# Kernel tuning notes

Measured on AMD Instinct MI355X. Metric: run time of the kernel, lower is better.

The kernel has to match this reference:

```python
import jax, jax.numpy as jnp
import numpy as np

EPS = 1e-6
NUM_HEADS = 12


def _layernorm(x, eps=EPS):
    m = jnp.mean(x, axis=-1, keepdims=True)
    v = jnp.var(x, axis=-1, keepdims=True)
    return (x - m) * jax.lax.rsqrt(v + eps)


def _rmsnorm(x, w, eps=EPS):
    ms = jnp.mean(jnp.square(x), axis=-1, keepdims=True)
    return x * jax.lax.rsqrt(ms + eps) * w


def _rope_interleaved(x, cos, sin):
    # x: [B, L, H, hd]; cos/sin: [L, hd//2]; is_neox_style=False (interleaved pairs)
    x1 = x[..., 0::2]
    x2 = x[..., 1::2]
    c = cos[None, :, None, :]
    s = sin[None, :, None, :]
    o1 = x1 * c - x2 * s
    o2 = x1 * s + x2 * c
    return jnp.stack([o1, o2], axis=-1).reshape(x.shape)


def _attention(q, k, v, mask=None):
    # q: [B, Lq, H, hd], k/v: [B, Lk, H, hd]
    hd = q.shape[-1]
    scale = 1.0 / jnp.sqrt(jnp.asarray(hd, q.dtype))
    scores = jnp.einsum('blhd,bmhd->bhlm', q, k) * scale
    if mask is not None:
        scores = jnp.where(mask[None, None], scores, jnp.finfo(scores.dtype).min)
    p = jax.nn.softmax(scores, axis=-1)
    return jnp.einsum('bhlm,bmhd->blhd', p, v)


def setup_inputs() -> dict:
    key = jax.random.key(0)
    B, F, FS, D, FF, LC = 1, 2, 1560, 1536, 8960, 512
    L = F * FS
    hd = D // NUM_HEADS
    ks = jax.random.split(key, 32)
    i = iter(range(32))
    n = lambda shape, s=0.02: jax.random.normal(ks[next(i)], shape, jnp.float32) * s
    inp = {
        'hidden_states': n((B, L, D), 1.0),
        'encoder_hidden_states': n((B, LC, D), 1.0),
        'temb': n((B, F, 6, D), 1.0),
    }
    pos = jnp.arange(L, dtype=jnp.float32)
    inv = 1.0 / (10000.0 ** (jnp.arange(hd // 2, dtype=jnp.float32) / (hd // 2)))
    ang = pos[:, None] * inv[None, :]
    inp['cos'] = jnp.cos(ang)
    inp['sin'] = jnp.sin(ang)
    fidx = jnp.arange(L) // FS
    inp['attn_mask'] = fidx[:, None] >= fidx[None, :]  # frame-level block-causal
    # params
    inp['sst'] = n((1, 6, D), 1.0 / np.sqrt(D))
    for name in ['wq', 'wk', 'wv', 'wo']:
        inp[name] = n((D, D))
    for name in ['bq', 'bk', 'bv', 'bo']:
        inp[name] = jnp.zeros((D,), jnp.float32)
    inp['nq_w'] = jnp.ones((D,), jnp.float32)
    inp['nk_w'] = jnp.ones((D,), jnp.float32)
    inp['ln2_g'] = jnp.ones((D,), jnp.float32)
    inp['ln2_b'] = jnp.zeros((D,), jnp.float32)
    for name in ['cwq', 'cwk', 'cwv', 'cwo']:
        inp[name] = n((D, D))
    for name in ['cbq', 'cbk', 'cbv', 'cbo']:
        inp[name] = jnp.zeros((D,), jnp.float32)
    inp['cnq_w'] = jnp.ones((D,), jnp.float32)
    inp['cnk_w'] = jnp.ones((D,), jnp.float32)
    inp['w1'] = n((D, FF))
    inp['b1'] = jnp.zeros((FF,), jnp.float32)
    inp['w2'] = n((FF, D))
    inp['b2'] = jnp.zeros((D,), jnp.float32)
    return inp


def reference(hidden_states, encoder_hidden_states, temb, cos, sin, attn_mask,
              sst, wq, bq, wk, bk, wv, bv, wo, bo, nq_w, nk_w, ln2_g, ln2_b,
              cwq, cbq, cwk, cbk, cwv, cbv, cwo, cbo, cnq_w, cnk_w,
              w1, b1, w2, b2):
    B, L, D = hidden_states.shape
    F = temb.shape[1]
    FS = L // F
    H = NUM_HEADS
    hd = D // H

    e = sst[:, None] + temb  # [B, F, 6, D]
    shift_msa, scale_msa, gate_msa = e[:, :, 0], e[:, :, 1], e[:, :, 2]
    c_shift, c_scale, c_gate = e[:, :, 3], e[:, :, 4], e[:, :, 5]

    # --- self attention ---
    nh = _layernorm(hidden_states).reshape(B, F, FS, D)
    nh = (nh * (1.0 + scale_msa[:, :, None]) + shift_msa[:, :, None]).reshape(B, L, D)
    q = _rmsnorm(nh @ wq + bq, nq_w).reshape(B, L, H, hd)
    k = _rmsnorm(nh @ wk + bk, nk_w).reshape(B, L, H, hd)
    v = (nh @ wv + bv).reshape(B, L, H, hd)
    q = _rope_interleaved(q, cos, sin)
    k = _rope_interleaved(k, cos, sin)
    attn_out = _attention(q, k, v, attn_mask).reshape(B, L, D) @ wo + bo

    h = hidden_states + (attn_out.reshape(B, F, FS, D) * gate_msa[:, :, None]).reshape(B, L, D)
    norm_h = _layernorm(h) * ln2_g + ln2_b  # null shift/scale

    # --- cross attention ---
    LC = encoder_hidden_states.shape[1]
    cq = _rmsnorm(norm_h @ cwq + cbq, cnq_w).reshape(B, L, H, hd)
    ck = _rmsnorm(encoder_hidden_states @ cwk + cbk, cnk_w).reshape(B, LC, H, hd)
    cv = (encoder_hidden_states @ cwv + cbv).reshape(B, LC, H, hd)
    cross_out = _attention(cq, ck, cv).reshape(B, L, D) @ cwo + cbo

    h = h + cross_out  # gate = 1
    norm_h = _layernorm(h).reshape(B, F, FS, D)
    norm_h = (norm_h * (1.0 + c_scale[:, :, None]) + c_shift[:, :, None]).reshape(B, L, D)

    # --- ffn ---
    ff = jax.nn.gelu(norm_h @ w1 + b1, approximate=True) @ w2 + b2
    h = h + (ff.reshape(B, F, FS, D) * c_gate[:, :, None]).reshape(B, L, D)
    return h
```

## Files before the change

kernel.cpp:

```cpp
#include <hip/hip_runtime.h>
#include <hip/hip_bf16.h>
#include <math.h>

typedef __bf16 bf16;
typedef __bf16 bf16x8 __attribute__((ext_vector_type(8)));
typedef float  f32x4  __attribute__((ext_vector_type(4)));
typedef unsigned int u32;

#define DMODEL 1536
#define NHEADS 12
#define HD 128
#define HDH 64

__device__ __forceinline__ void async16(const void* g, void* l) {
  __builtin_amdgcn_global_load_lds((const __attribute__((address_space(1))) u32*)g,
                                   (__attribute__((address_space(3))) u32*)l, 16, 0, 0);
}

__device__ inline void block_reduce2(float& a, float& b) {
  __shared__ float sa[4], sb[4];
  #pragma unroll
  for (int off = 32; off; off >>= 1) {
    a += __shfl_xor(a, off);
    b += __shfl_xor(b, off);
  }
  int w = threadIdx.x >> 6;
  if ((threadIdx.x & 63) == 0) { sa[w] = a; sb[w] = b; }
  __syncthreads();
  a = sa[0] + sa[1] + sa[2] + sa[3];
  b = sb[0] + sb[1] + sb[2] + sb[3];
  __syncthreads();
}

__global__ __launch_bounds__(256)
void ln_kernel(const float* __restrict__ X, bf16* __restrict__ Y,
               const float* __restrict__ sst, const float* __restrict__ temb,
               const float* __restrict__ g, const float* __restrict__ bvec,
               int jshift, int jscale, int FS, int mode)
{
  int row = blockIdx.x;
  const float* x = X + (size_t)row * DMODEL;
  float v[6];
  float s1 = 0.f, s2 = 0.f;
  #pragma unroll
  for (int i = 0; i < 6; i++) {
    float t = x[threadIdx.x + i * 256];
    v[i] = t; s1 += t; s2 += t * t;
  }
  block_reduce2(s1, s2);
  float mean = s1 * (1.f / DMODEL);
  float var  = s2 * (1.f / DMODEL) - mean * mean;
  float rs = rsqrtf(var + 1e-6f);
  int f = row / FS;
  bf16* y = Y + (size_t)row * DMODEL;
  #pragma unroll
  for (int i = 0; i < 6; i++) {
    int d = threadIdx.x + i * 256;
    float t = (v[i] - mean) * rs;
    float o;
    if (mode == 0) {
      float sc = sst[jscale * DMODEL + d] + temb[(f * 6 + jscale) * DMODEL + d];
      float sh = sst[jshift * DMODEL + d] + temb[(f * 6 + jshift) * DMODEL + d];
      o = t * (1.f + sc) + sh;
    } else {
      o = t * g[d] + bvec[d];
    }
    y[d] = (bf16)o;
  }
}

__global__ __launch_bounds__(256)
void rms_rope_kernel(const float* __restrict__ P, int S, long long MN,
                     const bf16* __restrict__ Xb, int RS, int CO,
                     const float* __restrict__ bias, bf16* __restrict__ Y,
                     const float* __restrict__ w,
                     const float* __restrict__ cosb, const float* __restrict__ sinb,
                     int dorope, float oscale)
{
  __shared__ float rowbuf[DMODEL];
  int row = blockIdx.x;
  float v[6];
  float s2 = 0.f, dummy = 0.f;
  if (Xb) {
    const bf16* x = Xb + (size_t)row * RS + CO;
    #pragma unroll
    for (int i = 0; i < 6; i++) {
      int d = threadIdx.x + i * 256;
      float t = (float)x[d];
      v[i] = t; rowbuf[d] = t; s2 += t * t;
    }
  } else {
    const float* x = P + (size_t)row * RS + CO;
    #pragma unroll
    for (int i = 0; i < 6; i++) {
      int d = threadIdx.x + i * 256;
      float t = bias[d];
      for (int s = 0; s < S; s++) t += x[(size_t)s * MN + d];
      v[i] = t; rowbuf[d] = t; s2 += t * t;
    }
  }
  __syncthreads();
  block_reduce2(s2, dummy);
  float rs = rsqrtf(s2 * (1.f / DMODEL) + 1e-6f) * oscale;
  bf16* y = Y + (size_t)row * DMODEL;
  if (dorope) {
    #pragma unroll
    for (int i = 0; i < 3; i++) {
      int p = threadIdx.x + i * 256;
      int d0 = 2 * p, d1 = 2 * p + 1;
      float y0 = rowbuf[d0] * rs * w[d0];
      float y1 = rowbuf[d1] * rs * w[d1];
      int ih = p & 63;
      float c = cosb[(size_t)row * HDH + ih];
      float s = sinb[(size_t)row * HDH + ih];
      y[d0] = (bf16)(y0 * c - y1 * s);
      y[d1] = (bf16)(y0 * s + y1 * c);
    }
  } else {
    #pragma unroll
    for (int i = 0; i < 6; i++) {
      int d = threadIdx.x + i * 256;
      y[d] = (bf16)(v[i] * rs * w[d]);
    }
  }
}

__global__ __launch_bounds__(256)
void wt_kernel(const float* __restrict__ W, bf16* __restrict__ Wt, int K, int N)
{
  __shared__ float T[32][33];
  int k0 = blockIdx.x * 32, n0 = blockIdx.y * 32;
  int tx = threadIdx.x & 31, ty = threadIdx.x >> 5;
  #pragma unroll
  for (int i = 0; i < 4; i++)
    T[ty + 8 * i][tx] = W[(size_t)(k0 + ty + 8 * i) * N + n0 + tx];
  __syncthreads();
  #pragma unroll
  for (int i = 0; i < 4; i++)
    Wt[(size_t)(n0 + ty + 8 * i) * K + k0 + tx] = (bf16)T[tx][ty + 8 * i];
}

__global__ __launch_bounds__(256)
void catbias_kernel(float* __restrict__ bqkv, const float* __restrict__ bq,
                    const float* __restrict__ bk, const float* __restrict__ bv,
                    float* __restrict__ cbkv, const float* __restrict__ cbk,
                    const float* __restrict__ cbv)
{
  int i = blockIdx.x * 256 + threadIdx.x;
  if (i < DMODEL) {
    bqkv[i] = bq[i]; bqkv[DMODEL + i] = bk[i]; bqkv[2 * DMODEL + i] = bv[i];
    cbkv[i] = cbk[i]; cbkv[DMODEL + i] = cbv[i];
  }
}

__global__ __launch_bounds__(256)
void gemm_bt(const bf16* __restrict__ A, const bf16* __restrict__ Bt,
             const float* __restrict__ bias, float* __restrict__ Cf,
             bf16* __restrict__ Cb, int M, int N, int K, int act,
             int Ks, long long MN)
{
  __shared__ bf16 As[128 * 32];
  __shared__ bf16 Bs[128 * 32];
  int tid = threadIdx.x, lane = tid & 63, w = tid >> 6;
  int wm = w >> 1, wn = w & 1;
  int l16 = lane & 15, quad = lane >> 4;

  int gx = (M + 127) >> 7, gy = N >> 7;
  int per_panel = gx << 3;
  int bid = blockIdx.x;
  int panel = bid / per_panel;
  int rem = bid - panel * per_panel;
  int pc0 = panel << 3;
  int ncols = gy - pc0; if (ncols > 8) ncols = 8;
  int by = pc0 + rem % ncols;
  int bx = rem / ncols;
  int bm = bx * 128, bn = by * 128;

  int kb0 = blockIdx.y * Ks;

  int rl = lane >> 2;
  int kk = (lane & 3) * 8;
  int r0 = (2 * w) * 16 + rl, r1 = (2 * w + 1) * 16 + rl;
  int am0 = bm + r0; if (am0 > M - 1) am0 = M - 1;
  int am1 = bm + r1; if (am1 > M - 1) am1 = M - 1;
  const bf16* a0 = A + (size_t)am0 * K + kk;
  const bf16* a1 = A + (size_t)am1 * K + kk;
  const bf16* b0 = Bt + (size_t)(bn + r0) * K + kk;
  const bf16* b1 = Bt + (size_t)(bn + r1) * K + kk;
  bf16* lA0 = As + (2 * w) * 512; bf16* lA1 = As + (2 * w + 1) * 512;
  bf16* lB0 = Bs + (2 * w) * 512; bf16* lB1 = Bs + (2 * w + 1) * 512;

  f32x4 acc[4][4] = {};
  int kend = kb0 + Ks;
  for (int k0 = kb0; k0 < kend; k0 += 32) {
    async16(a0 + k0, lA0);
    async16(a1 + k0, lA1);
    async16(b0 + k0, lB0);
    async16(b1 + k0, lB1);
    __syncthreads();
    bf16x8 af[4], bfv[4];
    #pragma unroll
    for (int mi = 0; mi < 4; mi++)
      af[mi] = *(const bf16x8*)&As[(wm * 64 + mi * 16 + l16) * 32 + quad * 8];
    #pragma unroll
    for (int ni = 0; ni < 4; ni++)
      bfv[ni] = *(const bf16x8*)&Bs[(wn * 64 + ni * 16 + l16) * 32 + quad * 8];
    #pragma unroll
    for (int mi = 0; mi < 4; mi++)
      #pragma unroll
      for (int ni = 0; ni < 4; ni++)
        acc[mi][ni] = __builtin_amdgcn_mfma_f32_16x16x32_bf16(af[mi], bfv[ni], acc[mi][ni], 0, 0, 0);
    __syncthreads();
  }
  float* Cfo = Cf ? Cf + (size_t)blockIdx.y * MN : nullptr;
  #pragma unroll
  for (int mi = 0; mi < 4; mi++) {
    #pragma unroll
    for (int r = 0; r < 4; r++) {
      int m = bm + wm * 64 + mi * 16 + quad * 4 + r;
      if (m < M) {
        #pragma unroll
        for (int ni = 0; ni < 4; ni++) {
          int n = bn + wn * 64 + ni * 16 + l16;
          float val = acc[mi][ni][r] + (bias ? bias[n] : 0.f);
          if (act == 1) {
            float u = val + 0.044715f * val * val * val;
            float z = 1.5957691216057308f * u;
            val = val / (1.f + __expf(-z));
          }
          if (Cfo) Cfo[(size_t)m * N + n] = val;
          else     Cb[(size_t)m * N + n] = (bf16)val;
        }
      }
    }
  }
}

__global__ __launch_bounds__(512, 2)
void gemm256(const bf16* __restrict__ A, const bf16* __restrict__ Bt,
             const float* __restrict__ bias, float* __restrict__ Cf,
             bf16* __restrict__ Cb, int M, int N, int K, int act,
             int S, long long MN)
{
  __shared__ bf16 LDS[4][2][16 * 512];
  int tid = threadIdx.x, lane = tid & 63, w = tid >> 6;
  int wm = w >> 2, wn = w & 3;
  int l16 = lane & 15, quad = lane >> 4;

  int gmx = (M + 255) >> 8, gny = N >> 8;
  int per_panel = gmx << 3;
  int bid = blockIdx.x;
  int panel = bid / per_panel;
  int rem = bid - panel * per_panel;
  int pc0 = panel << 3;
  int ncols = gny - pc0; if (ncols > 8) ncols = 8;
  int by = pc0 + rem % ncols;
  int bx = rem / ncols;
  int bm = bx << 8, bn = by << 8;

  int NTtot = K >> 5;
  int sidx = blockIdx.y;
  int basek = NTtot / S, remk = NTtot % S;
  int NT = basek + (sidx < remk ? 1 : 0);
  int t0k = sidx * basek + (sidx < remk ? sidx : remk);
  int kb0 = t0k << 5;

  int aro = (l16 * 64 + quad * 16) ^ ((l16 >> 3) << 5);
  char* ldsb = (char*)&LDS[0][0][0];

  int srl = lane >> 2;
  int sc16 = (lane & 3) ^ (((lane >> 5) & 1) << 1);
  int Mm1 = M - 1, Nm1 = N - 1;
  int ga0 = bm + w * 16 + srl;        if (ga0 > Mm1) ga0 = Mm1;
  int ga1 = bm + 128 + w * 16 + srl;  if (ga1 > Mm1) ga1 = Mm1;
  int gb0 = bn + w * 16 + srl;        if (gb0 > Nm1) gb0 = Nm1;
  int gb1 = bn + 128 + w * 16 + srl;  if (gb1 > Nm1) gb1 = Nm1;
  const bf16* Ag0 = A + (size_t)ga0 * K + kb0 + sc16 * 8;
  const bf16* Ag1 = A + (size_t)ga1 * K + kb0 + sc16 * 8;
  const bf16* Bg0 = Bt + (size_t)gb0 * K + kb0 + sc16 * 8;
  const bf16* Bg1 = Bt + (size_t)gb1 * K + kb0 + sc16 * 8;

#define STG(tt) do { int _k = (tt) * 32; char* _d = ldsb + ((tt) & 3) * 32768 + w * 1024; \
    async16(Ag0 + _k, _d);          async16(Ag1 + _k, _d + 8192); \
    async16(Bg0 + _k, _d + 16384);  async16(Bg1 + _k, _d + 24576); } while (0)
#define MFMA_(d, a, b) d = __builtin_amdgcn_mfma_f32_16x16x32_bf16(a, b, d, 0, 0, 0)

  STG(0);
  if (NT > 1) STG(1);
  if (NT > 2) STG(2);
  if (NT > 2)      { asm volatile("s_waitcnt vmcnt(8)" ::: "memory"); }
  else if (NT > 1) { asm volatile("s_waitcnt vmcnt(4)" ::: "memory"); }
  else             { asm volatile("s_waitcnt vmcnt(0)" ::: "memory"); }
  __builtin_amdgcn_s_barrier();

  f32x4 acc[8][4] = {};
  for (int t = 0; t < NT; ++t) {
    if (t + 3 < NT) STG(t + 3);
    const char* Ar = ldsb + (t & 3) * 32768 + wm * 8192 + aro;
    const char* Br = ldsb + (t & 3) * 32768 + 16384 + wn * 4096 + aro;
    bf16x8 a[8], bv[4];
    #pragma unroll
    for (int i = 0; i < 4; i++) bv[i] = *(const bf16x8*)(Br + i * 1024);
    #pragma unroll
    for (int i = 0; i < 8; i++) a[i] = *(const bf16x8*)(Ar + i * 1024);
    #pragma unroll
    for (int mi = 0; mi < 8; mi++)
      #pragma unroll
      for (int ni = 0; ni < 4; ni++)
        MFMA_(acc[mi][ni], a[mi], bv[ni]);
    int remt = NT - 1 - t;
    if (remt >= 3)      { asm volatile("s_waitcnt vmcnt(8)" ::: "memory"); __builtin_amdgcn_s_barrier(); }
    else if (remt == 2) { asm volatile("s_waitcnt vmcnt(4)" ::: "memory"); __builtin_amdgcn_s_barrier(); }
    else if (remt == 1) { asm volatile("s_waitcnt vmcnt(0)" ::: "memory"); __builtin_amdgcn_s_barrier(); }
  }
#undef STG
#undef MFMA_

  float* Cfo = Cf ? Cf + (size_t)blockIdx.y * MN : nullptr;
  #pragma unroll
  for (int mi = 0; mi < 8; mi++) {
    #pragma unroll
    for (int r = 0; r < 4; r++) {
      int m = bm + wm * 128 + mi * 16 + quad * 4 + r;
      if (m < M) {
        #pragma unroll
        for (int ni = 0; ni < 4; ni++) {
          int n = bn + wn * 64 + ni * 16 + l16;
          float val = acc[mi][ni][r] + (bias ? bias[n] : 0.f);
          if (act == 1) {
            float u = val + 0.044715f * val * val * val;
            float z = 1.5957691216057308f * u;
            val = val / (1.f + __expf(-z));
          }
          if (Cfo) Cfo[(size_t)m * N + n] = val;
          else     Cb[(size_t)m * N + n] = (bf16)val;
        }
      }
    }
  }
}

__global__ __launch_bounds__(256)
void transposev_kernel(const bf16* __restrict__ Xb, int RS, int CO,
                       bf16* __restrict__ Vt, int L)
{
  __shared__ bf16 T[64][65];
  int l0 = blockIdx.x * 64, n0 = blockIdx.y * 64;
  int tid = threadIdx.x;
  int r = tid >> 2;
  int c8 = (tid & 3) * 16;
  int lc = l0 + r; if (lc > L - 1) lc = L - 1;
  const bf16* src = Xb + (size_t)lc * RS + CO + n0 + c8;
  #pragma unroll
  for (int i = 0; i < 16; i++) T[r][c8 + i] = src[i];
  __syncthreads();
  #pragma unroll
  for (int i = 0; i < 16; i++) {
    int l = l0 + c8 + i;
    if (l < L) Vt[(size_t)(n0 + r) * L + l] = T[c8 + i][r];
  }
}

__global__ __launch_bounds__(256)
void flash2_kernel(const bf16* __restrict__ Q, const bf16* __restrict__ Kg,
                   const bf16* __restrict__ Vt, bf16* __restrict__ O,
                   int Lq, int Lk, int FS, int causal, int nqb)
{
  __shared__ bf16 Kt[64 * 128];
  __shared__ bf16 Vtile[128 * 64];
  __shared__ bf16 Pl[4][16][72];
  int tid = threadIdx.x, lane = tid & 63, w = tid >> 6;
  int l16 = lane & 15, quad = lane >> 4;
  int bid = blockIdx.x;
  int h = bid % NHEADS;
  int qb = nqb - 1 - (bid / NHEADS);
  int q0b = qb * 64;
  int q0w = q0b + w * 16;

  int qrow = q0w + l16; if (qrow > Lq - 1) qrow = Lq - 1;
  const bf16* qbase = Q + (size_t)qrow * DMODEL + h * HD + quad * 8;
  bf16x8 qf[4];
  #pragma unroll
  for (int dc = 0; dc < 4; dc++) qf[dc] = *(const bf16x8*)(qbase + dc * 32);

  int kvrow[4];
  int kvmin_w = Lk, kv_end = Lk;
  if (causal) {
    #pragma unroll
    for (int r = 0; r < 4; r++) {
      int qr = q0w + quad * 4 + r; if (qr > Lq - 1) qr = Lq - 1;
      kvrow[r] = (qr / FS + 1) * FS;
    }
    int q0c = q0w; if (q0c > Lq - 1) q0c = Lq - 1;
    kvmin_w = (q0c / FS + 1) * FS;
    int qlast = q0b + 63; if (qlast > Lq - 1) qlast = Lq - 1;
    kv_end = (qlast / FS + 1) * FS;
    if (kv_end > Lk) kv_end = Lk;
  }

  f32x4 acc_o[8] = {};
  float m_i[4], l_i[4];
  #pragma unroll
  for (int r = 0; r < 4; r++) { m_i[r] = -1e30f; l_i[r] = 0.f; }

  for (int kb = 0; kb < kv_end; kb += 64) {
    #pragma unroll
    for (int j = 0; j < 4; j++) {
      int u = w * 256 + j * 64 + lane;
      int row = u >> 4;
      int c = (u & 15) ^ (row & 15);
      int krow = kb + row; if (krow > Lk - 1) krow = Lk - 1;
      async16(Kg + (size_t)krow * DMODEL + h * HD + c * 8,
              Kt + (size_t)(w * 256 + j * 64) * 8);
    }
    #pragma unroll
    for (int j = 0; j < 4; j++) {
      int u = w * 256 + j * 64 + lane;
      int row = u >> 3;
      int c = (u & 7) ^ (row & 7);
      async16(Vt + (size_t)(h * HD + row) * Lk + kb + c * 8,
              Vtile + (size_t)(w * 256 + j * 64) * 8);
    }
    __syncthreads();

    f32x4 s[4] = {};
    #pragma unroll
    for (int nk = 0; nk < 4; nk++) {
      #pragma unroll
      for (int dc = 0; dc < 4; dc++) {
        bf16x8 kf = *(const bf16x8*)&Kt[(((nk * 16 + l16) << 4) + ((4 * dc + quad) ^ l16)) * 8];
        s[nk] = __builtin_amdgcn_mfma_f32_16x16x32_bf16(qf[dc], kf, s[nk], 0, 0, 0);
      }
    }

    bool need_mask = causal && (kb + 64 > kvmin_w);
    float p[4][4];
    #pragma unroll
    for (int r = 0; r < 4; r++) {
      #pragma unroll
      for (int nk = 0; nk < 4; nk++) {
        float sv = s[nk][r];
        if (need_mask && (kb + nk * 16 + l16 >= kvrow[r])) sv = -1e30f;
        p[nk][r] = sv;
      }
      float bm = fmaxf(fmaxf(p[0][r], p[1][r]), fmaxf(p[2][r], p[3][r]));
      #pragma unroll
      for (int off = 8; off; off >>= 1) bm = fmaxf(bm, __shfl_xor(bm, off));
      float mn = fmaxf(m_i[r], bm);
      float alpha = __expf(m_i[r] - mn);
      m_i[r] = mn;
      float ps = 0.f;
      #pragma unroll
      for (int nk = 0; nk < 4; nk++) {
        float e = __expf(p[nk][r] - mn);
        p[nk][r] = e; ps += e;
      }
      #pragma unroll
      for (int off = 8; off; off >>= 1) ps += __shfl_xor(ps, off);
      l_i[r] = l_i[r] * alpha + ps;
      #pragma unroll
      for (int t = 0; t < 8; t++) acc_o[t][r] *= alpha;
    }

    #pragma unroll
    for (int nk = 0; nk < 4; nk++)
      #pragma unroll
      for (int r = 0; r < 4; r++)
        Pl[w][quad * 4 + r][nk * 16 + l16] = (bf16)p[nk][r];
    __threadfence_block();
    bf16x8 pf0 = *(const bf16x8*)&Pl[w][l16][quad * 8];
    bf16x8 pf1 = *(const bf16x8*)&Pl[w][l16][32 + quad * 8];

    #pragma unroll
    for (int t = 0; t < 8; t++) {
      bf16x8 vf0 = *(const bf16x8*)&Vtile[(((t * 16 + l16) << 3) + ((quad) ^ (l16 & 7))) * 8];
      bf16x8 vf1 = *(const bf16x8*)&Vtile[(((t * 16 + l16) << 3) + ((4 + quad) ^ (l16 & 7))) * 8];
      acc_o[t] = __builtin_amdgcn_mfma_f32_16x16x32_bf16(pf0, vf0, acc_o[t], 0, 0, 0);
      acc_o[t] = __builtin_amdgcn_mfma_f32_16x16x32_bf16(pf1, vf1, acc_o[t], 0, 0, 0);
    }
    __syncthreads();
  }

  #pragma unroll
  for (int r = 0; r < 4; r++) {
    int m = q0w + quad * 4 + r;
    if (m < Lq) {
      float inv = 1.f / l_i[r];
      bf16* obase = O + (size_t)m * DMODEL + h * HD;
      #pragma unroll
      for (int t = 0; t < 8; t++)
        obase[t * 16 + l16] = (bf16)(acc_o[t][r] * inv);
    }
  }
}

__global__ __launch_bounds__(256)
void modresid_kernel(const float* __restrict__ base, const float* __restrict__ P,
                     int S, long long MN, const float* __restrict__ bias,
                     float* __restrict__ out,
                     const float* __restrict__ sst, const float* __restrict__ temb,
                     int jg, int FS, long long total)
{
  long long i = (long long)blockIdx.x * 256 + threadIdx.x;
  if (i >= total) return;
  int d = (int)(i % DMODEL);
  int f = (int)((i / DMODEL) / FS);
  float g = sst[jg * DMODEL + d] + temb[(f * 6 + jg) * DMODEL + d];
  float v = bias[d];
  for (int s = 0; s < S; s++) v += P[(size_t)s * MN + i];
  out[i] = base[i] + v * g;
}

__global__ __launch_bounds__(256)
void addf_kernel(float* __restrict__ h, const float* __restrict__ P,
                 int S, long long MN, const float* __restrict__ bias, long long total)
{
  long long i = (long long)blockIdx.x * 256 + threadIdx.x;
  if (i >= total) return;
  int d = (int)(i % DMODEL);
  float v = bias[d];
  for (int s = 0; s < S; s++) v += P[(size_t)s * MN + i];
  h[i] += v;
}

__global__ __launch_bounds__(256)
void cast_kernel(const float* __restrict__ x, bf16* __restrict__ y, long long total)
{
  long long i = (long long)blockIdx.x * 256 + threadIdx.x;
  if (i < total) y[i] = (bf16)x[i];
}

extern "C" void kernel_launch(void* const* d_in, const int* in_sizes, int n_in,
                              void* d_out, int out_size, void* d_ws, size_t ws_size,
                              hipStream_t stream)
{
  const float* hs   = (const float*)d_in[0];
  const float* enc  = (const float*)d_in[1];
  const float* temb = (const float*)d_in[2];
  const float* cosb = (const float*)d_in[3];
  const float* sinb = (const float*)d_in[4];
  const float* sst  = (const float*)d_in[6];
  const float* wq = (const float*)d_in[7];
  const float* wk = (const float*)d_in[8];
  const float* wv = (const float*)d_in[9];
  const float* wo = (const float*)d_in[10];
  const float* bq = (const float*)d_in[11];
  const float* bk = (const float*)d_in[12];
  const float* bv = (const float*)d_in[13];
  const float* bo = (const float*)d_in[14];
  const float* nq_w = (const float*)d_in[15];
  const float* nk_w = (const float*)d_in[16];
  const float* ln2_g = (const float*)d_in[17];
  const float* ln2_b = (const float*)d_in[18];
  const float* cwq = (const float*)d_in[19];
  const float* cwk = (const float*)d_in[20];
  const float* cwv = (const float*)d_in[21];
  const float* cwo = (const float*)d_in[22];
  const float* cbq = (const float*)d_in[23];
  const float* cbk = (const float*)d_in[24];
  const float* cbv = (const float*)d_in[25];
  const float* cbo = (const float*)d_in[26];
  const float* cnq_w = (const float*)d_in[27];
  const float* cnk_w = (const float*)d_in[28];
  const float* w1 = (const float*)d_in[29];
  const float* b1 = (const float*)d_in[30];
  const float* w2 = (const float*)d_in[31];
  const float* b2 = (const float*)d_in[32];

  int L  = in_sizes[0] / DMODEL;
  int LC = in_sizes[1] / DMODEL;
  int F  = in_sizes[2] / (6 * DMODEL);
  int FS = L / F;
  int FF = in_sizes[30];
  long long LD = (long long)L * DMODEL;
  float* outp = (float*)d_out;
  int N3 = 3 * DMODEL, N2 = 2 * DMODEL;

  char* p = (char*)d_ws;
  auto alloc = [&](size_t bytes) -> char* {
    char* r = p; p += (bytes + 255) & ~(size_t)255; return r;
  };
  size_t DD = (size_t)DMODEL * DMODEL;
  bf16* wqkv_t = (bf16*)alloc(DD * 3 * 2);
  bf16* wto_t  = (bf16*)alloc(DD * 2);
  bf16* cwq_t  = (bf16*)alloc(DD * 2);
  bf16* cwkv_t = (bf16*)alloc(DD * 2 * 2);
  bf16* cwo_t  = (bf16*)alloc(DD * 2);
  bf16* w1t = (bf16*)alloc((size_t)DMODEL * FF * 2);
  bf16* w2t = (bf16*)alloc((size_t)DMODEL * FF * 2);
  float* bqkv = (float*)alloc((size_t)N3 * 4);
  float* cbkv = (float*)alloc((size_t)N2 * 4);
  float* hbuf = (float*)alloc((size_t)LD * 4);
  bf16* nh   = (bf16*)alloc((size_t)LD * 2);
  bf16* qb   = (bf16*)alloc((size_t)LD * 2);
  bf16* kb   = (bf16*)alloc((size_t)LD * 2);
  bf16* ab   = (bf16*)alloc((size_t)LD * 2);
  bf16* vtc  = (bf16*)alloc((size_t)LC * DMODEL * 2);
  bf16* encb = (bf16*)alloc((size_t)LC * DMODEL * 2);
  char* BIG1 = alloc((size_t)L * FF * 2);
  bf16* qkvb = (bf16*)BIG1;
  bf16* ckvb = (bf16*)BIG1;
  bf16* ffb  = (bf16*)BIG1;
  char* BIG2 = alloc((size_t)LD * 3 * 4);
  bf16* vtb = (bf16*)BIG2;
  float* Pp = (float*)BIG2;
  (void)ws_size; (void)n_in; (void)out_size;

  dim3 gWdd(DMODEL / 32, DMODEL / 32);
  wt_kernel<<<gWdd, 256, 0, stream>>>(wq, wqkv_t, DMODEL, DMODEL);
  wt_kernel<<<gWdd, 256, 0, stream>>>(wk, wqkv_t + DD, DMODEL, DMODEL);
  wt_kernel<<<gWdd, 256, 0, stream>>>(wv, wqkv_t + 2 * DD, DMODEL, DMODEL);
  wt_kernel<<<gWdd, 256, 0, stream>>>(wo, wto_t, DMODEL, DMODEL);
  wt_kernel<<<gWdd, 256, 0, stream>>>(cwq, cwq_t, DMODEL, DMODEL);
  wt_kernel<<<gWdd, 256, 0, stream>>>(cwk, cwkv_t, DMODEL, DMODEL);
  wt_kernel<<<gWdd, 256, 0, stream>>>(cwv, cwkv_t + DD, DMODEL, DMODEL);
  wt_kernel<<<gWdd, 256, 0, stream>>>(cwo, cwo_t, DMODEL, DMODEL);
  wt_kernel<<<dim3(DMODEL / 32, FF / 32), 256, 0, stream>>>(w1, w1t, DMODEL, FF);
  wt_kernel<<<dim3(FF / 32, DMODEL / 32), 256, 0, stream>>>(w2, w2t, FF, DMODEL);
  catbias_kernel<<<6, 256, 0, stream>>>(bqkv, bq, bk, bv, cbkv, cbk, cbv);

  int gxC = (LC + 127) / 128;
  int gmx = (L + 255) / 256;
  int ewg = (int)((LD + 255) / 256);
  int nqb = (L + 63) / 64;
  const float qs = 0.08838834764831845f;

  ln_kernel<<<L, 256, 0, stream>>>(hs, nh, sst, temb, nullptr, nullptr, 0, 1, FS, 0);
  gemm256<<<dim3(gmx * (N3 / 256), 1), 512, 0, stream>>>(nh, wqkv_t, bqkv, nullptr, qkvb,
                                                         L, N3, DMODEL, 0, 1, 0);
  rms_rope_kernel<<<L, 256, 0, stream>>>(nullptr, 0, 0, qkvb, N3, 0, nullptr, qb, nq_w, cosb, sinb, 1, qs);
  rms_rope_kernel<<<L, 256, 0, stream>>>(nullptr, 0, 0, qkvb, N3, DMODEL, nullptr, kb, nk_w, cosb, sinb, 1, 1.0f);
  transposev_kernel<<<dim3((L + 63) / 64, DMODEL / 64), 256, 0, stream>>>(qkvb, N3, 2 * DMODEL, vtb, L);
  flash2_kernel<<<NHEADS * nqb, 256, 0, stream>>>(qb, kb, vtb, ab, L, L, FS, 1, nqb);
  gemm256<<<dim3(gmx * (DMODEL / 256), 3), 512, 0, stream>>>(ab, wto_t, nullptr, Pp, nullptr,
                                                             L, DMODEL, DMODEL, 0, 3, LD);
  modresid_kernel<<<ewg, 256, 0, stream>>>(hs, Pp, 3, LD, bo, hbuf, sst, temb, 2, FS, LD);
  ln_kernel<<<L, 256, 0, stream>>>(hbuf, nh, nullptr, nullptr, ln2_g, ln2_b, 0, 0, FS, 1);
  gemm256<<<dim3(gmx * (DMODEL / 256), 3), 512, 0, stream>>>(nh, cwq_t, nullptr, Pp, nullptr,
                                                             L, DMODEL, DMODEL, 0, 3, LD);
  rms_rope_kernel<<<L, 256, 0, stream>>>(Pp, 3, LD, nullptr, DMODEL, 0, cbq, qb, cnq_w, nullptr, nullptr, 0, qs);
  cast_kernel<<<(int)(((long long)LC * DMODEL + 255) / 256), 256, 0, stream>>>(enc, encb, (long long)LC * DMODEL);
  gemm_bt<<<dim3(gxC * (N2 / 128), 1), 256, 0, stream>>>(encb, cwkv_t, cbkv, nullptr, ckvb,
                                                         LC, N2, DMODEL, 0, DMODEL, 0);
  rms_rope_kernel<<<LC, 256, 0, stream>>>(nullptr, 0, 0, ckvb, N2, 0, nullptr, kb, cnk_w, nullptr, nullptr, 0, 1.0f);
  transposev_kernel<<<dim3((LC + 63) / 64, DMODEL / 64), 256, 0, stream>>>(ckvb, N2, DMODEL, vtc, LC);
  flash2_kernel<<<NHEADS * nqb, 256, 0, stream>>>(qb, kb, vtc, ab, L, LC, FS, 0, nqb);
  gemm256<<<dim3(gmx * (DMODEL / 256), 3), 512, 0, stream>>>(ab, cwo_t, nullptr, Pp, nullptr,
                                                             L, DMODEL, DMODEL, 0, 3, LD);
  addf_kernel<<<ewg, 256, 0, stream>>>(hbuf, Pp, 3, LD, cbo, LD);
  ln_kernel<<<L, 256, 0, stream>>>(hbuf, nh, sst, temb, nullptr, nullptr, 3, 4, FS, 0);
  gemm256<<<dim3(gmx * (FF / 256), 1), 512, 0, stream>>>(nh, w1t, b1, nullptr, ffb,
                                                         L, FF, DMODEL, 1, 1, 0);
  gemm256<<<dim3(gmx * (DMODEL / 256), 3), 512, 0, stream>>>(ffb, w2t, nullptr, Pp, nullptr,
                                                             L, DMODEL, FF, 0, 3, LD);
  modresid_kernel<<<ewg, 256, 0, stream>>>(hbuf, Pp, 3, LD, b2, outp, sst, temb, 5, FS, LD);
}
```

Baseline: 1.092 ms.

## Fuse residual+layernorm and q/k rmsnorm-rope kernels; widen flash attention q-tile

Merges the split-K residual reduction with the following layernorm into per-row kernels, so the hidden state is no longer written and then re-read. Q and K RMSNorm+RoPE now run in one launch instead of two. The flash attention kernel uses 512 threads covering 128 query rows per block, so each K/V tile loaded into LDS is reused by twice as many rows. The cost is fewer attention blocks and possibly lower occupancy, plus coarser causal bounds per block that may compute more masked work.

```diff
diff --git a/kernel.cpp b/kernel.cpp
--- a/kernel.cpp
+++ b/kernel.cpp
@@ -35,8 +35,7 @@
 __global__ __launch_bounds__(256)
 void ln_kernel(const float* __restrict__ X, bf16* __restrict__ Y,
                const float* __restrict__ sst, const float* __restrict__ temb,
-               const float* __restrict__ g, const float* __restrict__ bvec,
-               int jshift, int jscale, int FS, int mode)
+               int jshift, int jscale, int FS)
 {
   int row = blockIdx.x;
   const float* x = X + (size_t)row * DMODEL;
@@ -57,15 +56,9 @@
   for (int i = 0; i < 6; i++) {
     int d = threadIdx.x + i * 256;
     float t = (v[i] - mean) * rs;
-    float o;
-    if (mode == 0) {
-      float sc = sst[jscale * DMODEL + d] + temb[(f * 6 + jscale) * DMODEL + d];
-      float sh = sst[jshift * DMODEL + d] + temb[(f * 6 + jshift) * DMODEL + d];
-      o = t * (1.f + sc) + sh;
-    } else {
-      o = t * g[d] + bvec[d];
-    }
-    y[d] = (bf16)o;
+    float sc = sst[jscale * DMODEL + d] + temb[(f * 6 + jscale) * DMODEL + d];
+    float sh = sst[jshift * DMODEL + d] + temb[(f * 6 + jshift) * DMODEL + d];
+    y[d] = (bf16)(t * (1.f + sc) + sh);
   }
 }
 
@@ -122,6 +115,46 @@
       int d = threadIdx.x + i * 256;
       y[d] = (bf16)(v[i] * rs * w[d]);
     }
+  }
+}
+
+__global__ __launch_bounds__(256)
+void rmsrope_qk_kernel(const bf16* __restrict__ Xb, int RS,
+                       bf16* __restrict__ Q, bf16* __restrict__ Kb,
+                       const float* __restrict__ wq, const float* __restrict__ wk,
+                       const float* __restrict__ cosb, const float* __restrict__ sinb,
+                       float qscale)
+{
+  __shared__ float rowbuf[DMODEL];
+  int row = blockIdx.x;
+  for (int pass = 0; pass < 2; ++pass) {
+    const bf16* x = Xb + (size_t)row * RS + (pass ? DMODEL : 0);
+    const float* wv = pass ? wk : wq;
+    bf16* y = (pass ? Kb : Q) + (size_t)row * DMODEL;
+    float osc = pass ? 1.0f : qscale;
+    float s2 = 0.f, dmy = 0.f;
+    #pragma unroll
+    for (int i = 0; i < 6; i++) {
+      int d = threadIdx.x + i * 256;
+      float t = (float)x[d];
+      rowbuf[d] = t; s2 += t * t;
+    }
+    __syncthreads();
+    block_reduce2(s2, dmy);
+    float rs = rsqrtf(s2 * (1.f / DMODEL) + 1e-6f) * osc;
+    #pragma unroll
+    for (int i = 0; i < 3; i++) {
+      int p = threadIdx.x + i * 256;
+      int d0 = 2 * p, d1 = 2 * p + 1;
+      float y0 = rowbuf[d0] * rs * wv[d0];
+      float y1 = rowbuf[d1] * rs * wv[d1];
+      int ih = p & 63;
+      float c = cosb[(size_t)row * HDH + ih];
+      float s = sinb[(size_t)row * HDH + ih];
+      y[d0] = (bf16)(y0 * c - y1 * s);
+      y[d1] = (bf16)(y0 * s + y1 * c);
+    }
+    __syncthreads();
   }
 }
 
@@ -361,20 +394,20 @@
   }
 }
 
-__global__ __launch_bounds__(256)
+__global__ __launch_bounds__(512)
 void flash2_kernel(const bf16* __restrict__ Q, const bf16* __restrict__ Kg,
                    const bf16* __restrict__ Vt, bf16* __restrict__ O,
                    int Lq, int Lk, int FS, int causal, int nqb)
 {
   __shared__ bf16 Kt[64 * 128];
   __shared__ bf16 Vtile[128 * 64];
-  __shared__ bf16 Pl[4][16][72];
+  __shared__ bf16 Pl[8][16][72];
   int tid = threadIdx.x, lane = tid & 63, w = tid >> 6;
   int l16 = lane & 15, quad = lane >> 4;
   int bid = blockIdx.x;
   int h = bid % NHEADS;
   int qb = nqb - 1 - (bid / NHEADS);
-  int q0b = qb * 64;
+  int q0b = qb * 128;
   int q0w = q0b + w * 16;
 
   int qrow = q0w + l16; if (qrow > Lq - 1) qrow = Lq - 1;
@@ -393,7 +426,7 @@
     }
     int q0c = q0w; if (q0c > Lq - 1) q0c = Lq - 1;
     kvmin_w = (q0c / FS + 1) * FS;
-    int qlast = q0b + 63; if (qlast > Lq - 1) qlast = Lq - 1;
+    int qlast = q0b + 127; if (qlast > Lq - 1) qlast = Lq - 1;
     kv_end = (qlast / FS + 1) * FS;
     if (kv_end > Lk) kv_end = Lk;
   }
@@ -405,21 +438,21 @@
 
   for (int kb = 0; kb < kv_end; kb += 64) {
     #pragma unroll
-    for (int j = 0; j < 4; j++) {
-      int u = w * 256 + j * 64 + lane;
+    for (int j = 0; j < 2; j++) {
+      int u = w * 128 + j * 64 + lane;
       int row = u >> 4;
       int c = (u & 15) ^ (row & 15);
       int krow = kb + row; if (krow > Lk - 1) krow = Lk - 1;
       async16(Kg + (size_t)krow * DMODEL + h * HD + c * 8,
-              Kt + (size_t)(w * 256 + j * 64) * 8);
-    }
-    #pragma unroll
-    for (int j = 0; j < 4; j++) {
-      int u = w * 256 + j * 64 + lane;
+              Kt + (size_t)(w * 128 + j * 64) * 8);
+    }
+    #pragma unroll
+    for (int j = 0; j < 2; j++) {
+      int u = w * 128 + j * 64 + lane;
       int row = u >> 3;
       int c = (u & 7) ^ (row & 7);
       async16(Vt + (size_t)(h * HD + row) * Lk + kb + c * 8,
-              Vtile + (size_t)(w * 256 + j * 64) * 8);
+              Vtile + (size_t)(w * 128 + j * 64) * 8);
     }
     __syncthreads();
 
@@ -491,6 +524,75 @@
       for (int t = 0; t < 8; t++)
         obase[t * 16 + l16] = (bf16)(acc_o[t][r] * inv);
     }
+  }
+}
+
+__global__ __launch_bounds__(256)
+void modresid_ln_kernel(const float* __restrict__ base, const float* __restrict__ P,
+                        int S, long long MN, const float* __restrict__ bias,
+                        float* __restrict__ hout,
+                        const float* __restrict__ sst, const float* __restrict__ temb,
+                        int jg, int FS,
+                        const float* __restrict__ g2, const float* __restrict__ b2,
+                        bf16* __restrict__ nh)
+{
+  int row = blockIdx.x;
+  int f = row / FS;
+  float v[6]; float s1 = 0.f, s2 = 0.f;
+  #pragma unroll
+  for (int i = 0; i < 6; i++) {
+    int d = threadIdx.x + i * 256;
+    long long idx = (size_t)row * DMODEL + d;
+    float gg = sst[jg * DMODEL + d] + temb[(f * 6 + jg) * DMODEL + d];
+    float t = bias[d];
+    for (int s = 0; s < S; s++) t += P[(size_t)s * MN + idx];
+    float hv = base[idx] + t * gg;
+    hout[idx] = hv;
+    v[i] = hv; s1 += hv; s2 += hv * hv;
+  }
+  block_reduce2(s1, s2);
+  float mean = s1 * (1.f / DMODEL);
+  float var  = s2 * (1.f / DMODEL) - mean * mean;
+  float rs = rsqrtf(var + 1e-6f);
+  bf16* y = nh + (size_t)row * DMODEL;
+  #pragma unroll
+  for (int i = 0; i < 6; i++) {
+    int d = threadIdx.x + i * 256;
+    y[d] = (bf16)((v[i] - mean) * rs * g2[d] + b2[d]);
+  }
+}
+
+__global__ __launch_bounds__(256)
+void addf_ln_kernel(float* __restrict__ hbuf, const float* __restrict__ P,
+                    int S, long long MN, const float* __restrict__ bias,
+                    const float* __restrict__ sst, const float* __restrict__ temb,
+                    int jshift, int jscale, int FS, bf16* __restrict__ nh)
+{
+  int row = blockIdx.x;
+  int f = row / FS;
+  float v[6]; float s1 = 0.f, s2 = 0.f;
+  #pragma unroll
+  for (int i = 0; i < 6; i++) {
+    int d = threadIdx.x + i * 256;
+    long long idx = (size_t)row * DMODEL + d;
+    float t = bias[d];
+    for (int s = 0; s < S; s++) t += P[(size_t)s * MN + idx];
+    float hv = hbuf[idx] + t;
+    hbuf[idx] = hv;
+    v[i] = hv; s1 += hv; s2 += hv * hv;
+  }
+  block_reduce2(s1, s2);
+  float mean = s1 * (1.f / DMODEL);
+  float var  = s2 * (1.f / DMODEL) - mean * mean;
+  float rs = rsqrtf(var + 1e-6f);
+  bf16* y = nh + (size_t)row * DMODEL;
+  #pragma unroll
+  for (int i = 0; i < 6; i++) {
+    int d = threadIdx.x + i * 256;
+    float t = (v[i] - mean) * rs;
+    float sc = sst[jscale * DMODEL + d] + temb[(f * 6 + jscale) * DMODEL + d];
+    float sh = sst[jshift * DMODEL + d] + temb[(f * 6 + jshift) * DMODEL + d];
+    y[d] = (bf16)(t * (1.f + sc) + sh);
   }
 }
 
@@ -509,18 +611,6 @@
   float v = bias[d];
   for (int s = 0; s < S; s++) v += P[(size_t)s * MN + i];
   out[i] = base[i] + v * g;
-}
-
-__global__ __launch_bounds__(256)
-void addf_kernel(float* __restrict__ h, const float* __restrict__ P,
-                 int S, long long MN, const float* __restrict__ bias, long long total)
-{
-  long long i = (long long)blockIdx.x * 256 + threadIdx.x;
-  if (i >= total) return;
-  int d = (int)(i % DMODEL);
-  float v = bias[d];
-  for (int s = 0; s < S; s++) v += P[(size_t)s * MN + i];
-  h[i] += v;
 }
 
 __global__ __launch_bounds__(256)
@@ -621,21 +711,19 @@
 
   int gxC = (LC + 127) / 128;
   int gmx = (L + 255) / 256;
-  int ewg = (int)((LD + 255) / 256);
-  int nqb = (L + 63) / 64;
+  int nqb = (L + 127) / 128;
   const float qs = 0.08838834764831845f;
 
-  ln_kernel<<<L, 256, 0, stream>>>(hs, nh, sst, temb, nullptr, nullptr, 0, 1, FS, 0);
+  ln_kernel<<<L, 256, 0, stream>>>(hs, nh, sst, temb, 0, 1, FS);
   gemm256<<<dim3(gmx * (N3 / 256), 1), 512, 0, stream>>>(nh, wqkv_t, bqkv, nullptr, qkvb,
                                                          L, N3, DMODEL, 0, 1, 0);
-  rms_rope_kernel<<<L, 256, 0, stream>>>(nullptr, 0, 0, qkvb, N3, 0, nullptr, qb, nq_w, cosb, sinb, 1, qs);
-  rms_rope_kernel<<<L, 256, 0, stream>>>(nullptr, 0, 0, qkvb, N3, DMODEL, nullptr, kb, nk_w, cosb, sinb, 1, 1.0f);
+  rmsrope_qk_kernel<<<L, 256, 0, stream>>>(qkvb, N3, qb, kb, nq_w, nk_w, cosb, sinb, qs);
   transposev_kernel<<<dim3((L + 63) / 64, DMODEL / 64), 256, 0, stream>>>(qkvb, N3, 2 * DMODEL, vtb, L);
-  flash2_kernel<<<NHEADS * nqb, 256, 0, stream>>>(qb, kb, vtb, ab, L, L, FS, 1, nqb);
+  flash2_kernel<<<NHEADS * nqb, 512, 0, stream>>>(qb, kb, vtb, ab, L, L, FS, 1, nqb);
   gemm256<<<dim3(gmx * (DMODEL / 256), 3), 512, 0, stream>>>(ab, wto_t, nullptr, Pp, nullptr,
                                                              L, DMODEL, DMODEL, 0, 3, LD);
-  modresid_kernel<<<ewg, 256, 0, stream>>>(hs, Pp, 3, LD, bo, hbuf, sst, temb, 2, FS, LD);
-  ln_kernel<<<L, 256, 0, stream>>>(hbuf, nh, nullptr, nullptr, ln2_g, ln2_b, 0, 0, FS, 1);
+  modresid_ln_kernel<<<L, 256, 0, stream>>>(hs, Pp, 3, LD, bo, hbuf, sst, temb, 2, FS,
+                                            ln2_g, ln2_b, nh);
   gemm256<<<dim3(gmx * (DMODEL / 256), 3), 512, 0, stream>>>(nh, cwq_t, nullptr, Pp, nullptr,
                                                              L, DMODEL, DMODEL, 0, 3, LD);
   rms_rope_kernel<<<L, 256, 0, stream>>>(Pp, 3, LD, nullptr, DMODEL, 0, cbq, qb, cnq_w, nullptr, nullptr, 0, qs);
@@ -644,14 +732,13 @@
                                                          LC, N2, DMODEL, 0, DMODEL, 0);
   rms_rope_kernel<<<LC, 256, 0, stream>>>(nullptr, 0, 0, ckvb, N2, 0, nullptr, kb, cnk_w, nullptr, nullptr, 0, 1.0f);
   transposev_kernel<<<dim3((LC + 63) / 64, DMODEL / 64), 256, 0, stream>>>(ckvb, N2, DMODEL, vtc, LC);
-  flash2_kernel<<<NHEADS * nqb, 256, 0, stream>>>(qb, kb, vtc, ab, L, LC, FS, 0, nqb);
+  flash2_kernel<<<NHEADS * nqb, 512, 0, stream>>>(qb, kb, vtc, ab, L, LC, FS, 0, nqb);
   gemm256<<<dim3(gmx * (DMODEL / 256), 3), 512, 0, stream>>>(ab, cwo_t, nullptr, Pp, nullptr,
                                                              L, DMODEL, DMODEL, 0, 3, LD);
-  addf_kernel<<<ewg, 256, 0, stream>>>(hbuf, Pp, 3, LD, cbo, LD);
-  ln_kernel<<<L, 256, 0, stream>>>(hbuf, nh, sst, temb, nullptr, nullptr, 3, 4, FS, 0);
+  addf_ln_kernel<<<L, 256, 0, stream>>>(hbuf, Pp, 3, LD, cbo, sst, temb, 3, 4, FS, nh);
   gemm256<<<dim3(gmx * (FF / 256), 1), 512, 0, stream>>>(nh, w1t, b1, nullptr, ffb,
                                                          L, FF, DMODEL, 1, 1, 0);
   gemm256<<<dim3(gmx * (DMODEL / 256), 3), 512, 0, stream>>>(ffb, w2t, nullptr, Pp, nullptr,
                                                              L, DMODEL, FF, 0, 3, LD);
-  modresid_kernel<<<ewg, 256, 0, stream>>>(hbuf, Pp, 3, LD, b2, outp, sst, temb, 5, FS, LD);
-}
+  modresid_kernel<<<(int)((LD + 255) / 256), 256, 0, stream>>>(hbuf, Pp, 3, LD, b2, outp, sst, temb, 5, FS, LD);
+}
```

Measured after the change: 1.113 ms. Within noise of the previous version (+1.9%).
